# Performance work log

Hardware: AMD Instinct MI355X
Metric: run time of the kernel (lower is better)

Reference implementation:

```python
import jax, jax.numpy as jnp
import numpy as np

N_NODES = 50000
N_EDGES = 800000
D = 128


def setup_inputs() -> dict:
    key = jax.random.key(0)
    ks = jax.random.split(key, 7)
    return {
        "shape_features": jax.random.normal(ks[0], (N_NODES, D), dtype=jnp.float32),
        "W1": jax.random.normal(ks[1], (D, D), dtype=jnp.float32) * 0.05,
        "b1": jax.random.normal(ks[2], (D,), dtype=jnp.float32) * 0.05,
        "W2": jax.random.normal(ks[3], (D, D), dtype=jnp.float32) * 0.05,
        "b2": jax.random.normal(ks[4], (D,), dtype=jnp.float32) * 0.05,
        "edge_src": jax.random.randint(ks[5], (N_EDGES,), 0, N_NODES, dtype=jnp.int32),
        "edge_dst": jax.random.randint(ks[6], (N_EDGES,), 0, N_NODES, dtype=jnp.int32),
    }


def reference(shape_features, W1, b1, W2, b2, edge_src, edge_dst):
    # out1 = linear1(x)  (torch Linear: x @ W.T + b)
    out1 = jnp.einsum("nd,od->no", shape_features, W1) + b1
    # ragged neighbour gather + sum per destination node (segment reduce)
    aggr = jax.ops.segment_sum(shape_features[edge_src], edge_dst,
                               num_segments=shape_features.shape[0])
    # out = linear1(x) + linear2(aggr)
    return out1 + jnp.einsum("nd,od->no", aggr, W2) + b2
```

## Files before the change

kernel.cpp:

```cpp
#include <hip/hip_runtime.h>
#include <hip/hip_bf16.h>

#define DF 128
#define BSH 5
#define BNODES 32
#define NBMAX 2048
#define CHUNK 8192
#define TILE 2048
#define ASTRIDE 68
#define SRCMASK 0x07ffffffu

typedef __attribute__((ext_vector_type(8))) short short8;
typedef __attribute__((ext_vector_type(4))) float floatx4;

__device__ __forceinline__ ushort f2bf(float f) {
    __hip_bfloat16 h = __float2bfloat16(f);
    return *reinterpret_cast<ushort*>(&h);
}

__global__ __launch_bounds__(256) void prep_kernel(
    const float* __restrict__ x, ushort* __restrict__ xbf, int n4,
    const float* __restrict__ W1, const float* __restrict__ W2,
    const float* __restrict__ b1, const float* __restrict__ b2,
    ushort* __restrict__ w1bf, ushort* __restrict__ w2bf, float* __restrict__ bias,
    const int* __restrict__ dst, int* __restrict__ histG,
    int n_edges, int B_, int nb)
{
    __shared__ int h[NBMAX];
    int bid = blockIdx.x;
    if (bid < B_) {
        for (int j = threadIdx.x; j < nb; j += 256) h[j] = 0;
        __syncthreads();
        int base = bid * CHUNK;
#pragma unroll 4
        for (int i = 0; i < CHUNK / 256; ++i) {
            int e = base + i * 256 + threadIdx.x;
            if (e < n_edges) atomicAdd(&h[dst[e] >> BSH], 1);
        }
        __syncthreads();
        for (int j = threadIdx.x; j < nb; j += 256)
            histG[j * B_ + bid] = h[j];
    } else if (bid < B_ + 64) {
        int i = (bid - B_) * 256 + threadIdx.x;
        if (i < DF * DF) {
            w1bf[i] = f2bf(W1[i]);
            w2bf[i] = f2bf(W2[i]);
        }
        if (i < DF) bias[i] = b1[i] + b2[i];
    } else {
        int i = (bid - B_ - 64) * 256 + threadIdx.x;
        if (i < n4) {
            float4 v = reinterpret_cast<const float4*>(x)[i];
            ushort4 o;
            o.x = f2bf(v.x); o.y = f2bf(v.y); o.z = f2bf(v.z); o.w = f2bf(v.w);
            reinterpret_cast<ushort4*>(xbf)[i] = o;
        }
    }
}

__global__ __launch_bounds__(256) void scan_local_kernel(
    const int* __restrict__ cnt, int* __restrict__ offs,
    int* __restrict__ bsum, int n)
{
    __shared__ int sd[256];
    int t = threadIdx.x;
    int base = blockIdx.x * 1024 + t * 4;

    int4 v = make_int4(0, 0, 0, 0);
    if (base + 3 < n) {
        v = *reinterpret_cast<const int4*>(cnt + base);
    } else {
        if (base + 0 < n) v.x = cnt[base + 0];
        if (base + 1 < n) v.y = cnt[base + 1];
        if (base + 2 < n) v.z = cnt[base + 2];
        if (base + 3 < n) v.w = cnt[base + 3];
    }
    int s = v.x + v.y + v.z + v.w;
    sd[t] = s;
    __syncthreads();
    for (int off = 1; off < 256; off <<= 1) {
        int u = (t >= off) ? sd[t - off] : 0;
        __syncthreads();
        sd[t] += u;
        __syncthreads();
    }
    int incl = sd[t];
    int excl = incl - s;
    if (t == 255) bsum[blockIdx.x] = incl;

    int p0 = excl, p1 = p0 + v.x, p2 = p1 + v.y, p3 = p2 + v.z;
    if (base + 0 < n) offs[base + 0] = p0;
    if (base + 1 < n) offs[base + 1] = p1;
    if (base + 2 < n) offs[base + 2] = p2;
    if (base + 3 < n) offs[base + 3] = p3;
}

__global__ __launch_bounds__(1024) void scan_bsum_kernel(
    int* __restrict__ bsum, int nb2)
{
    __shared__ int sd[1024];
    int t = threadIdx.x;
    int v = (t < nb2) ? bsum[t] : 0;
    sd[t] = v;
    __syncthreads();
    for (int off = 1; off < 1024; off <<= 1) {
        int u = (t >= off) ? sd[t - off] : 0;
        __syncthreads();
        sd[t] += u;
        __syncthreads();
    }
    if (t < nb2) bsum[t] = sd[t] - v;
}

__global__ __launch_bounds__(256) void bin_kernel(
    const int* __restrict__ src, const int* __restrict__ dst,
    const int* __restrict__ histS, const int* __restrict__ bsum,
    uint* __restrict__ pairs, int n_edges, int B_, int nb)
{
    __shared__ int cur[NBMAX];
    int blk = blockIdx.x;
    for (int j = threadIdx.x; j < nb; j += 256) {
        int idx = j * B_ + blk;
        cur[j] = histS[idx] + bsum[idx >> 10];
    }
    __syncthreads();
    int base = blk * CHUNK;
#pragma unroll 4
    for (int i = 0; i < CHUNK / 256; ++i) {
        int e = base + i * 256 + threadIdx.x;
        if (e < n_edges) {
            int d = dst[e];
            int j = d >> BSH;
            int p = atomicAdd(&cur[j], 1);
            pairs[p] = (uint)src[e] | ((uint)(d & (BNODES - 1)) << 27);
        }
    }
}

__global__ __launch_bounds__(256) void agg_gemm_kernel(
    const ushort* __restrict__ xbf, const uint* __restrict__ pairs,
    const int* __restrict__ histS, const int* __restrict__ bsum,
    const ushort* __restrict__ w1, const ushort* __restrict__ w2,
    const float* __restrict__ bias, float* __restrict__ out,
    int n_nodes, int n_edges, int B_, int nb, int flat)
{
    __shared__ uint sorted[TILE];
    __shared__ uint abuf[BNODES * ASTRIDE];
    __shared__ int hcnt[BNODES];
    __shared__ int hoff[BNODES + 1];
    __shared__ int hcur[BNODES];

    int blk  = blockIdx.x;
    int node0 = blk * BNODES;
    int wave = threadIdx.x >> 6;
    int lane = threadIdx.x & 63;

    auto loadOffs = [&](int idx) -> int {
        if (idx >= flat) return n_edges;
        return histS[idx] + bsum[idx >> 10];
    };

    int e0 = loadOffs(blk * B_);
    int e1 = loadOffs((blk + 1) * B_);

    const uint* xv = reinterpret_cast<const uint*>(xbf);
    float2 acc[8];
#pragma unroll
    for (int i = 0; i < 8; ++i) acc[i] = make_float2(0.f, 0.f);

    for (int t0 = e0; t0 < e1; t0 += TILE) {
        int cnt = e1 - t0; if (cnt > TILE) cnt = TILE;

        if (threadIdx.x < BNODES) hcnt[threadIdx.x] = 0;
        __syncthreads();

        for (int i = threadIdx.x; i < cnt; i += 256)
            atomicAdd(&hcnt[pairs[t0 + i] >> 27], 1);
        __syncthreads();

        if (threadIdx.x < 64) {
            int v = (lane < BNODES) ? hcnt[lane] : 0;
#pragma unroll
            for (int off = 1; off < BNODES; off <<= 1) {
                int u = __shfl_up(v, off);
                if (lane >= off) v += u;
            }
            if (lane < BNODES) {
                hoff[lane + 1] = v;
                hcur[lane] = v - hcnt[lane];
            }
            if (lane == 0) hoff[0] = 0;
        }
        __syncthreads();

        for (int i = threadIdx.x; i < cnt; i += 256) {
            uint pk = pairs[t0 + i];
            int p = atomicAdd(&hcur[pk >> 27], 1);
            sorted[p] = pk & SRCMASK;
        }
        __syncthreads();

#pragma unroll
        for (int i = 0; i < 8; ++i) {
            int nl = wave * 8 + i;
            int j0 = hoff[nl], j1 = hoff[nl + 1];
            float2 a = acc[i];
            int j = j0;
            for (; j + 7 < j1; j += 8) {
                uint u0 = xv[(size_t)sorted[j + 0] * 64 + lane];
                uint u1 = xv[(size_t)sorted[j + 1] * 64 + lane];
                uint u2 = xv[(size_t)sorted[j + 2] * 64 + lane];
                uint u3 = xv[(size_t)sorted[j + 3] * 64 + lane];
                uint u4 = xv[(size_t)sorted[j + 4] * 64 + lane];
                uint u5 = xv[(size_t)sorted[j + 5] * 64 + lane];
                uint u6 = xv[(size_t)sorted[j + 6] * 64 + lane];
                uint u7 = xv[(size_t)sorted[j + 7] * 64 + lane];
                a.x += __uint_as_float(u0 << 16) + __uint_as_float(u1 << 16)
                     + __uint_as_float(u2 << 16) + __uint_as_float(u3 << 16)
                     + __uint_as_float(u4 << 16) + __uint_as_float(u5 << 16)
                     + __uint_as_float(u6 << 16) + __uint_as_float(u7 << 16);
                a.y += __uint_as_float(u0 & 0xffff0000u) + __uint_as_float(u1 & 0xffff0000u)
                     + __uint_as_float(u2 & 0xffff0000u) + __uint_as_float(u3 & 0xffff0000u)
                     + __uint_as_float(u4 & 0xffff0000u) + __uint_as_float(u5 & 0xffff0000u)
                     + __uint_as_float(u6 & 0xffff0000u) + __uint_as_float(u7 & 0xffff0000u);
            }
            for (; j + 3 < j1; j += 4) {
                uint u0 = xv[(size_t)sorted[j + 0] * 64 + lane];
                uint u1 = xv[(size_t)sorted[j + 1] * 64 + lane];
                uint u2 = xv[(size_t)sorted[j + 2] * 64 + lane];
                uint u3 = xv[(size_t)sorted[j + 3] * 64 + lane];
                a.x += __uint_as_float(u0 << 16) + __uint_as_float(u1 << 16)
                     + __uint_as_float(u2 << 16) + __uint_as_float(u3 << 16);
                a.y += __uint_as_float(u0 & 0xffff0000u) + __uint_as_float(u1 & 0xffff0000u)
                     + __uint_as_float(u2 & 0xffff0000u) + __uint_as_float(u3 & 0xffff0000u);
            }
            for (; j < j1; ++j) {
                uint u = xv[(size_t)sorted[j] * 64 + lane];
                a.x += __uint_as_float(u << 16);
                a.y += __uint_as_float(u & 0xffff0000u);
            }
            acc[i] = a;
        }
        __syncthreads();
    }

#pragma unroll
    for (int i = 0; i < 8; ++i) {
        int nl = wave * 8 + i;
        abuf[nl * ASTRIDE + lane] =
            (uint)f2bf(acc[i].x) | ((uint)f2bf(acc[i].y) << 16);
    }
    __syncthreads();

    int quad = lane >> 4;
    int m    = lane & 15;
    int rg   = wave >> 1;
    int half = wave & 1;
    int rowL = rg * 16 + m;
    int rowG = node0 + rowL;
    int rowC = (rowG < n_nodes) ? rowG : (n_nodes - 1);

    short8 xa[4], aa[4];
#pragma unroll
    for (int ks = 0; ks < 4; ++ks) {
        xa[ks] = *reinterpret_cast<const short8*>(xbf + (size_t)rowC * DF + ks * 32 + quad * 8);
        aa[ks] = *reinterpret_cast<const short8*>(&abuf[rowL * ASTRIDE + ks * 16 + quad * 4]);
    }

    int nbase = node0 + rg * 16;
#pragma unroll
    for (int oi = 0; oi < 4; ++oi) {
        int ot = half * 4 + oi;
        int o = ot * 16 + m;
        floatx4 c = {0.f, 0.f, 0.f, 0.f};
#pragma unroll
        for (int ks = 0; ks < 4; ++ks) {
            short8 bf1 = *reinterpret_cast<const short8*>(w1 + (size_t)o * DF + ks * 32 + quad * 8);
            short8 bf2 = *reinterpret_cast<const short8*>(w2 + (size_t)o * DF + ks * 32 + quad * 8);
            c = __builtin_amdgcn_mfma_f32_16x16x32_bf16(xa[ks], bf1, c, 0, 0, 0);
            c = __builtin_amdgcn_mfma_f32_16x16x32_bf16(aa[ks], bf2, c, 0, 0, 0);
        }
        float bv = bias[o];
#pragma unroll
        for (int r = 0; r < 4; ++r) {
            int row = nbase + quad * 4 + r;
            if (row < n_nodes) out[(size_t)row * DF + o] = c[r] + bv;
        }
    }
}

extern "C" void kernel_launch(void* const* d_in, const int* in_sizes, int n_in,
                              void* d_out, int out_size, void* d_ws, size_t ws_size,
                              hipStream_t stream) {
    const float* x  = (const float*)d_in[0];
    const float* W1 = (const float*)d_in[1];
    const float* b1 = (const float*)d_in[2];
    const float* W2 = (const float*)d_in[3];
    const float* b2 = (const float*)d_in[4];
    const int* esrc = (const int*)d_in[5];
    const int* edst = (const int*)d_in[6];
    float* out = (float*)d_out;

    int n_nodes = in_sizes[0] / DF;
    int n_edges = in_sizes[5];

    int nb = (n_nodes + BNODES - 1) >> BSH;
    int B_ = (n_edges + CHUNK - 1) / CHUNK;
    int flat = nb * B_;

    char* ws = (char*)d_ws;
    ushort* xbf   = (ushort*)ws;                 ws += (size_t)n_nodes * DF * 2;
    ushort* w1bf  = (ushort*)ws;                 ws += (size_t)DF * DF * 2;
    ushort* w2bf  = (ushort*)ws;                 ws += (size_t)DF * DF * 2;
    float*  bias  = (float*)ws;                  ws += (size_t)DF * 4;
    int*    histG = (int*)ws;                    ws += (size_t)flat * 4;
    int*    histS = (int*)ws;                    ws += (size_t)(flat + 1) * 4;
    int*    bsum  = (int*)ws;                    ws += 1024 * 4;
    uint*   pairs = (uint*)ws;

    int n4 = n_nodes * DF / 4;
    int prep_blocks = B_ + 64 + (n4 + 255) / 256;
    prep_kernel<<<prep_blocks, 256, 0, stream>>>(
        x, xbf, n4, W1, W2, b1, b2, w1bf, w2bf, bias,
        edst, histG, n_edges, B_, nb);

    int nb2 = (flat + 1023) / 1024;
    scan_local_kernel<<<nb2, 256, 0, stream>>>(histG, histS, bsum, flat);
    scan_bsum_kernel<<<1, 1024, 0, stream>>>(bsum, nb2);

    bin_kernel<<<B_, 256, 0, stream>>>(esrc, edst, histS, bsum, pairs, n_edges, B_, nb);

    agg_gemm_kernel<<<nb, 256, 0, stream>>>(
        xbf, pairs, histS, bsum, w1bf, w2bf, bias, out,
        n_nodes, n_edges, B_, nb, flat);
}
```

Baseline: 179.8 us.

## Make binning block-major with LDS staging and coalesced pair writes

The histogram layout changes from bin-major to block-major, so each bin_kernel block sorts its chunk of edges locally in shared memory and writes its pairs back contiguously instead of scattering them across global memory. bin_kernel now runs 1024 threads per block. agg_gemm_kernel then gathers each bin's edges from up to B_ per-block runs: it computes run starts and lengths, prefix-sums them, and binary-searches to locate each edge. This trades scattered global writes in binning for extra index work and less contiguous reads in the aggregation kernel, and it assumes B_ <= 128.

```diff
diff --git a/kernel.cpp b/kernel.cpp
--- a/kernel.cpp
+++ b/kernel.cpp
@@ -6,6 +6,7 @@
 #define BNODES 32
 #define NBMAX 2048
 #define CHUNK 8192
+#define BMAX 128
 #define TILE 2048
 #define ASTRIDE 68
 #define SRCMASK 0x07ffffffu
@@ -39,7 +40,7 @@
         }
         __syncthreads();
         for (int j = threadIdx.x; j < nb; j += 256)
-            histG[j * B_ + bid] = h[j];
+            histG[bid * nb + j] = h[j];
     } else if (bid < B_ + 64) {
         int i = (bid - B_) * 256 + threadIdx.x;
         if (i < DF * DF) {
@@ -112,29 +113,31 @@
     if (t < nb2) bsum[t] = sd[t] - v;
 }
 
-__global__ __launch_bounds__(256) void bin_kernel(
+__global__ __launch_bounds__(1024) void bin_kernel(
     const int* __restrict__ src, const int* __restrict__ dst,
     const int* __restrict__ histS, const int* __restrict__ bsum,
     uint* __restrict__ pairs, int n_edges, int B_, int nb)
 {
-    __shared__ int cur[NBMAX];
+    __shared__ int  cur[NBMAX];
+    __shared__ uint stage[CHUNK];
     int blk = blockIdx.x;
-    for (int j = threadIdx.x; j < nb; j += 256) {
-        int idx = j * B_ + blk;
+    for (int j = threadIdx.x; j < nb; j += 1024) {
+        int idx = blk * nb + j;
         cur[j] = histS[idx] + bsum[idx >> 10];
     }
     __syncthreads();
     int base = blk * CHUNK;
-#pragma unroll 4
-    for (int i = 0; i < CHUNK / 256; ++i) {
-        int e = base + i * 256 + threadIdx.x;
-        if (e < n_edges) {
-            int d = dst[e];
-            int j = d >> BSH;
-            int p = atomicAdd(&cur[j], 1);
-            pairs[p] = (uint)src[e] | ((uint)(d & (BNODES - 1)) << 27);
-        }
-    }
+    int cnt = n_edges - base; if (cnt > CHUNK) cnt = CHUNK;
+    for (int i = threadIdx.x; i < cnt; i += 1024) {
+        int e = base + i;
+        int d = dst[e];
+        int j = d >> BSH;
+        int p = atomicAdd(&cur[j], 1);
+        stage[p - base] = (uint)src[e] | ((uint)(d & (BNODES - 1)) << 27);
+    }
+    __syncthreads();
+    for (int i = threadIdx.x; i < cnt; i += 1024)
+        pairs[base + i] = stage[i];
 }
 
 __global__ __launch_bounds__(256) void agg_gemm_kernel(
@@ -144,8 +147,11 @@
     const float* __restrict__ bias, float* __restrict__ out,
     int n_nodes, int n_edges, int B_, int nb, int flat)
 {
+    __shared__ uint raw[TILE];
     __shared__ uint sorted[TILE];
     __shared__ uint abuf[BNODES * ASTRIDE];
+    __shared__ int  rstart[BMAX];
+    __shared__ int  rexcl[BMAX + 1];
     __shared__ int hcnt[BNODES];
     __shared__ int hoff[BNODES + 1];
     __shared__ int hcur[BNODES];
@@ -160,22 +166,54 @@
         return histS[idx] + bsum[idx >> 10];
     };
 
-    int e0 = loadOffs(blk * B_);
-    int e1 = loadOffs((blk + 1) * B_);
+    if (threadIdx.x < B_) {
+        int idx = threadIdx.x * nb + blk;
+        int s = loadOffs(idx);
+        rstart[threadIdx.x] = s;
+        rexcl[threadIdx.x]  = loadOffs(idx + 1) - s;
+    }
+    __syncthreads();
+    if (threadIdx.x < 64) {
+        int c0 = (lane < B_) ? rexcl[lane] : 0;
+        int c1 = (64 + lane < B_) ? rexcl[64 + lane] : 0;
+        int s0 = c0, s1 = c1;
+#pragma unroll
+        for (int off = 1; off < 64; off <<= 1) {
+            int u0 = __shfl_up(s0, off);
+            int u1 = __shfl_up(s1, off);
+            if (lane >= off) { s0 += u0; s1 += u1; }
+        }
+        int t0 = __shfl(s0, 63);
+        int t1 = __shfl(s1, 63);
+        if (lane < B_) rexcl[lane] = s0 - c0;
+        if (64 + lane < B_) rexcl[64 + lane] = t0 + s1 - c1;
+        if (lane == 0) rexcl[B_] = t0 + t1;
+    }
+    __syncthreads();
+    int total = rexcl[B_];
 
     const uint* xv = reinterpret_cast<const uint*>(xbf);
     float2 acc[8];
 #pragma unroll
     for (int i = 0; i < 8; ++i) acc[i] = make_float2(0.f, 0.f);
 
-    for (int t0 = e0; t0 < e1; t0 += TILE) {
-        int cnt = e1 - t0; if (cnt > TILE) cnt = TILE;
+    for (int t0 = 0; t0 < total; t0 += TILE) {
+        int cnt = total - t0; if (cnt > TILE) cnt = TILE;
 
         if (threadIdx.x < BNODES) hcnt[threadIdx.x] = 0;
         __syncthreads();
 
-        for (int i = threadIdx.x; i < cnt; i += 256)
-            atomicAdd(&hcnt[pairs[t0 + i] >> 27], 1);
+        for (int i = threadIdx.x; i < cnt; i += 256) {
+            int t = t0 + i;
+            int lo = 0, hi = B_;
+            while (lo + 1 < hi) {
+                int mid = (lo + hi) >> 1;
+                if (rexcl[mid] <= t) lo = mid; else hi = mid;
+            }
+            uint pk = pairs[rstart[lo] + (t - rexcl[lo])];
+            raw[i] = pk;
+            atomicAdd(&hcnt[pk >> 27], 1);
+        }
         __syncthreads();
 
         if (threadIdx.x < 64) {
@@ -194,7 +232,7 @@
         __syncthreads();
 
         for (int i = threadIdx.x; i < cnt; i += 256) {
-            uint pk = pairs[t0 + i];
+            uint pk = raw[i];
             int p = atomicAdd(&hcur[pk >> 27], 1);
             sorted[p] = pk & SRCMASK;
         }
@@ -328,7 +366,7 @@
     scan_local_kernel<<<nb2, 256, 0, stream>>>(histG, histS, bsum, flat);
     scan_bsum_kernel<<<1, 1024, 0, stream>>>(bsum, nb2);
 
-    bin_kernel<<<B_, 256, 0, stream>>>(esrc, edst, histS, bsum, pairs, n_edges, B_, nb);
+    bin_kernel<<<B_, 1024, 0, stream>>>(esrc, edst, histS, bsum, pairs, n_edges, B_, nb);
 
     agg_gemm_kernel<<<nb, 256, 0, stream>>>(
         xbf, pairs, histS, bsum, w1bf, w2bf, bias, out,
```

Result: no change. 178.4 us (-0.8%).
